# Kernel optimization log

Measured on AMD Instinct MI355X. Metric: run time of the kernel, lower is better.

The kernel has to match this reference:

```python
import jax, jax.numpy as jnp
import numpy as np
from jax import lax

B, C, H, W = 2, 64, 64, 64


def _conv1x1(x, w, b):
    # w: [Cout, Cin], x: [B, Cin, H, W]
    return jnp.einsum('oi,bihw->bohw', w, x) + b[None, :, None, None]


def _conv3x3(x, w, b):
    # w: [Cout, Cin, 3, 3]
    y = lax.conv_general_dilated(x, w, (1, 1), 'SAME',
                                 dimension_numbers=('NCHW', 'OIHW', 'NCHW'))
    return y + b[None, :, None, None]


def _bn(x, s, b, m, v, eps=1e-5):
    # eval-mode batchnorm with running stats
    inv = s / jnp.sqrt(v + eps)
    return x * inv[None, :, None, None] + (b - m * inv)[None, :, None, None]


def _prelu(x, a):
    return jnp.where(x > 0, x, a * x)


def _forward(x, g,
             pam_q_w, pam_q_b, pam_k_w, pam_k_b, pam_v_w, pam_v_b,
             pam_qg_w, pam_qg_b, pam_kg_w, pam_kg_b, gamma_p,
             se_fc1_w, se_fc2_w, gamma_c,
             pconv1_w, pconv1_b, pbn1_s, pbn1_b, pbn1_m, pbn1_v, pprelu1,
             pconv2_w, pconv2_b, pbn2_s, pbn2_b, pbn2_m, pbn2_v, pprelu2,
             cconv1_w, cconv1_b, cbn1_s, cbn1_b, cbn1_m, cbn1_v, cprelu1,
             cconv2_w, cconv2_b, cbn2_s, cbn2_b, cbn2_m, cbn2_v, cprelu2,
             fconv_w, fconv_b, fbn_s, fbn_b, fbn_m, fbn_v, fprelu):
    b, c, h, w = x.shape
    n = h * w
    sm = jax.nn.softmax
    # ---- G_PAM: position attention with guided double softmax ----
    q = _conv1x1(x, pam_q_w, pam_q_b).reshape(b, c, n)
    k = _conv1x1(x, pam_k_w, pam_k_b).reshape(b, c, n)
    v = _conv1x1(x, pam_v_w, pam_v_b).reshape(b, c, n)
    qg = _conv1x1(g, pam_qg_w, pam_qg_b).reshape(b, -1, n)
    kg = _conv1x1(g, pam_kg_w, pam_kg_b).reshape(b, -1, n)
    att = sm(jnp.einsum('bcn,bcm->bnm', q, k), axis=-1)        # [B,N,N]
    att_g = sm(jnp.einsum('bcn,bcm->bnm', qg, kg), axis=-1)    # [B,N,N]
    gatt = sm(jnp.einsum('bnk,bkm->bnm', att, att_g), axis=-1) # [B,N,N]
    pam_o = jnp.einsum('bcm,bnm->bcn', v, gatt).reshape(b, c, h, w)
    pam = gamma_p * pam_o + x
    # ---- pconv head ----
    t = _prelu(_bn(_conv3x3(pam, pconv1_w, pconv1_b), pbn1_s, pbn1_b, pbn1_m, pbn1_v), pprelu1)
    pam2 = _prelu(_bn(_conv1x1(t, pconv2_w, pconv2_b), pbn2_s, pbn2_b, pbn2_m, pbn2_v), pprelu2)
    # ---- G_CAM: channel attention with SE-gated guide ----
    xq = pam2.reshape(b, c, n)
    att_c = sm(jnp.einsum('bcn,bdn->bcd', xq, xq), axis=-1)    # [B,C,C]
    gy = g.mean((2, 3))  # SE: [B,C]
    gy = jax.nn.sigmoid(jnp.einsum('oc,bc->bo', se_fc2_w,
                                   jax.nn.relu(jnp.einsum('rc,bc->br', se_fc1_w, gy))))
    gq = (g * gy[:, :, None, None]).reshape(b, c, n)
    att_cg = sm(jnp.einsum('bcn,bdn->bcd', gq, gq), axis=-1)   # [B,C,C]
    ge = jnp.einsum('bck,bkd->bcd', att_c, att_cg)
    ge = jnp.max(ge, axis=-1, keepdims=True) - ge
    gatt_c = sm(ge, axis=-1)
    cam_o = jnp.einsum('bcd,bdn->bcn', gatt_c, xq).reshape(b, c, h, w)
    cam = gamma_c * cam_o + pam2
    # ---- cconv + fconv heads ----
    t = _prelu(_bn(_conv3x3(cam, cconv1_w, cconv1_b), cbn1_s, cbn1_b, cbn1_m, cbn1_v), cprelu1)
    cam2 = _prelu(_bn(_conv1x1(t, cconv2_w, cconv2_b), cbn2_s, cbn2_b, cbn2_m, cbn2_v), cprelu2)
    final = _prelu(_bn(_conv1x1(cam2, fconv_w, fconv_b), fbn_s, fbn_b, fbn_m, fbn_v), fprelu)
    return final


def setup_inputs() -> dict:
    key = jax.random.key(0)
    keys = iter(jax.random.split(key, 64))
    nk = lambda: next(keys)
    f32 = jnp.float32
    nrm = lambda shape, s=0.1: s * jax.random.normal(nk(), shape, f32)
    d = {}
    d['x'] = jax.random.normal(nk(), (B, C, H, W), f32)
    d['g'] = jax.random.normal(nk(), (B, C, H, W), f32)
    for p in ['pam_q', 'pam_k', 'pam_v', 'pam_qg', 'pam_kg']:
        d[p + '_w'] = nrm((C, C))
        d[p + '_b'] = nrm((C,))
    d['gamma_p'] = jnp.asarray(0.5, f32)
    d['se_fc1_w'] = nrm((C // 2, C))
    d['se_fc2_w'] = nrm((C, C // 2))
    d['gamma_c'] = jnp.asarray(0.5, f32)
    for pre in ['p', 'c']:
        d[pre + 'conv1_w'] = nrm((C, C, 3, 3), 0.05)
        d[pre + 'conv1_b'] = nrm((C,))
        d[pre + 'bn1_s'] = 1.0 + nrm((C,))
        d[pre + 'bn1_b'] = nrm((C,))
        d[pre + 'bn1_m'] = nrm((C,))
        d[pre + 'bn1_v'] = 1.0 + 0.1 * jax.random.uniform(nk(), (C,), f32)
        d[pre + 'prelu1'] = jnp.asarray(0.25, f32)
        d[pre + 'conv2_w'] = nrm((C, C))
        d[pre + 'conv2_b'] = nrm((C,))
        d[pre + 'bn2_s'] = 1.0 + nrm((C,))
        d[pre + 'bn2_b'] = nrm((C,))
        d[pre + 'bn2_m'] = nrm((C,))
        d[pre + 'bn2_v'] = 1.0 + 0.1 * jax.random.uniform(nk(), (C,), f32)
        d[pre + 'prelu2'] = jnp.asarray(0.25, f32)
    d['fconv_w'] = nrm((C, C))
    d['fconv_b'] = nrm((C,))
    d['fbn_s'] = 1.0 + nrm((C,))
    d['fbn_b'] = nrm((C,))
    d['fbn_m'] = nrm((C,))
    d['fbn_v'] = 1.0 + 0.1 * jax.random.uniform(nk(), (C,), f32)
    d['fprelu'] = jnp.asarray(0.25, f32)
    return d


def reference(x, g,
              pam_q_w, pam_q_b, pam_k_w, pam_k_b, pam_v_w, pam_v_b,
              pam_qg_w, pam_qg_b, pam_kg_w, pam_kg_b, gamma_p,
              se_fc1_w, se_fc2_w, gamma_c,
              pconv1_w, pconv1_b, pbn1_s, pbn1_b, pbn1_m, pbn1_v, pprelu1,
              pconv2_w, pconv2_b, pbn2_s, pbn2_b, pbn2_m, pbn2_v, pprelu2,
              cconv1_w, cconv1_b, cbn1_s, cbn1_b, cbn1_m, cbn1_v, cprelu1,
              cconv2_w, cconv2_b, cbn2_s, cbn2_b, cbn2_m, cbn2_v, cprelu2,
              fconv_w, fconv_b, fbn_s, fbn_b, fbn_m, fbn_v, fprelu):
    return _forward(x, g,
                    pam_q_w, pam_q_b, pam_k_w, pam_k_b, pam_v_w, pam_v_b,
                    pam_qg_w, pam_qg_b, pam_kg_w, pam_kg_b, gamma_p,
                    se_fc1_w, se_fc2_w, gamma_c,
                    pconv1_w, pconv1_b, pbn1_s, pbn1_b, pbn1_m, pbn1_v, pprelu1,
                    pconv2_w, pconv2_b, pbn2_s, pbn2_b, pbn2_m, pbn2_v, pprelu2,
                    cconv1_w, cconv1_b, cbn1_s, cbn1_b, cbn1_m, cbn1_v, cprelu1,
                    cconv2_w, cconv2_b, cbn2_s, cbn2_b, cbn2_m, cbn2_v, cprelu2,
                    fconv_w, fconv_b, fbn_s, fbn_b, fbn_m, fbn_v, fprelu)
```

## Files before the change

### kernel.cpp

```cpp
#include <hip/hip_runtime.h>
#include <hip/hip_fp8.h>


typedef float f32x4 __attribute__((ext_vector_type(4)));
typedef __bf16 bf16x8 __attribute__((ext_vector_type(8)));
typedef int int4v __attribute__((ext_vector_type(4)));
typedef int int8v __attribute__((ext_vector_type(8)));
typedef unsigned short ushort8 __attribute__((ext_vector_type(8)));
typedef unsigned char uchar8 __attribute__((ext_vector_type(8)));

#define DI __device__ __forceinline__

DI float bf2f(unsigned short u) { union { unsigned int i; float f; } x; x.i = ((unsigned int)u) << 16; return x.f; }
DI unsigned short f2bf(float f) { union { float f; unsigned int i; } x; x.f = f; unsigned int r = x.i + 0x7fff + ((x.i >> 16) & 1); return (unsigned short)(r >> 16); }
DI unsigned char f2fp8(float f) { __hip_fp8_e4m3 h(f); return (unsigned char)h.__x; }
DI float sane(float x) { return (x > -1e8f) ? ((x < 1e8f) ? x : 1e8f) : -1e8f; }

DI void async16(const unsigned short* g, unsigned short* l) {
    __builtin_amdgcn_global_load_lds(
        (const __attribute__((address_space(1))) void*)g,
        (__attribute__((address_space(3))) void*)l, 16, 0, 0);
}
DI void async16b(const unsigned char* g, unsigned char* l) {
    __builtin_amdgcn_global_load_lds(
        (const __attribute__((address_space(1))) void*)g,
        (__attribute__((address_space(3))) void*)l, 16, 0, 0);
}

__global__ __launch_bounds__(256) void diag_fill(float* __restrict__ out, int n, float val)
{
    int i = blockIdx.x * 256 + threadIdx.x;
    if (i < n) out[i] = val;
}

__global__ __launch_bounds__(256) void gemm_score(
    const unsigned short* __restrict__ A,
    const unsigned short* __restrict__ B,
    unsigned short* __restrict__ C, int N, long abStride, long cStride)
{
    A += (long)blockIdx.z * abStride;
    B += (long)blockIdx.z * abStride;
    C += (long)blockIdx.z * cStride;
    const int tid  = threadIdx.x;
    const int bm   = blockIdx.y, bn = blockIdx.x;
    const int lane = tid & 63, wid = tid >> 6;
    const int wm   = (wid >> 1) * 64, wn = (wid & 1) * 64;
    const int l16  = lane & 15, quad = lane >> 4;

    f32x4 acc[4][4] = {};
    bf16x8 af[2][4], bfr[2][4];
    #pragma unroll
    for (int w = 0; w < 2; w++) {
        #pragma unroll
        for (int i = 0; i < 4; i++)
            af[w][i]  = *(const bf16x8*)&A[(long)(bm * 128 + wm + i * 16 + l16) * 64 + w * 32 + quad * 8];
        #pragma unroll
        for (int j = 0; j < 4; j++)
            bfr[w][j] = *(const bf16x8*)&B[(long)(bn * 128 + wn + j * 16 + l16) * 64 + w * 32 + quad * 8];
    }
    #pragma unroll
    for (int w = 0; w < 2; w++)
        #pragma unroll
        for (int i = 0; i < 4; i++)
            #pragma unroll
            for (int j = 0; j < 4; j++)
                acc[i][j] = __builtin_amdgcn_mfma_f32_16x16x32_bf16(af[w][i], bfr[w][j], acc[i][j], 0, 0, 0);

    #pragma unroll
    for (int i = 0; i < 4; i++) {
        int rb = bm * 128 + wm + i * 16 + quad * 4;
        #pragma unroll
        for (int j = 0; j < 4; j++) {
            int col = bn * 128 + wn + j * 16 + l16;
            #pragma unroll
            for (int r = 0; r < 4; r++)
                C[(long)(rb + r) * N + col] = f2bf(acc[i][j][r]);
        }
    }
}

__global__ __launch_bounds__(256, 3) void gemm_nt(
    const unsigned short* __restrict__ A,
    const unsigned short* __restrict__ B,
    float* __restrict__ C,
    int M, int N, int K, long sA, long sB, long sC)
{
    A += (long)blockIdx.z * sA;
    B += (long)blockIdx.z * sB;
    C += (long)blockIdx.z * sC;
    __shared__ __align__(16) unsigned short As[128 * 32];
    __shared__ __align__(16) unsigned short Bs[128 * 32];
    const int tid  = threadIdx.x;
    const int bn   = blockIdx.x, slice = blockIdx.y;
    const int lane = tid & 63, wid = tid >> 6;
    const int wm   = (wid >> 1) * 64, wn = (wid & 1) * 64;
    const int l16  = lane & 15, quad = lane >> 4;

    f32x4 acc[4][4] = {};

    const int Kc   = K / (int)gridDim.y;
    const int kbeg = slice * Kc;
    const int nIter = Kc / 32;

    const int row0 = tid >> 2,        cp0 = tid & 3;
    const int row1 = (tid + 256) >> 2, cp1 = (tid + 256) & 3;
    int ar0 = row0; if (ar0 > M - 1) ar0 = M - 1;
    int ar1 = row1; if (ar1 > M - 1) ar1 = M - 1;
    const unsigned short* pa0 = &A[(long)ar0 * K + kbeg + ((cp0 ^ (row0 & 3)) * 8)];
    const unsigned short* pa1 = &A[(long)ar1 * K + kbeg + ((cp1 ^ (row1 & 3)) * 8)];
    const unsigned short* pb0 = &B[(long)(bn * 128 + row0) * K + kbeg + ((cp0 ^ (row0 & 3)) * 8)];
    const unsigned short* pb1 = &B[(long)(bn * 128 + row1) * K + kbeg + ((cp1 ^ (row1 & 3)) * 8)];
    unsigned short* la0 = &As[row0 * 32 + cp0 * 8];
    unsigned short* la1 = &As[row1 * 32 + cp1 * 8];
    unsigned short* lb0 = &Bs[row0 * 32 + cp0 * 8];
    unsigned short* lb1 = &Bs[row1 * 32 + cp1 * 8];

    const int sw = (quad ^ (l16 & 3)) * 8;

    for (int it = 0; it < nIter; it++) {
        __syncthreads();
        async16(pa0, la0);
        async16(pa1, la1);
        async16(pb0, lb0);
        async16(pb1, lb1);
        pa0 += 32; pa1 += 32; pb0 += 32; pb1 += 32;
        __syncthreads();
        bf16x8 af[4], bfr[4];
        #pragma unroll
        for (int i = 0; i < 4; i++) af[i]  = *(const bf16x8*)&As[(wm + i * 16 + l16) * 32 + sw];
        #pragma unroll
        for (int j = 0; j < 4; j++) bfr[j] = *(const bf16x8*)&Bs[(wn + j * 16 + l16) * 32 + sw];
        #pragma unroll
        for (int i = 0; i < 4; i++)
            #pragma unroll
            for (int j = 0; j < 4; j++)
                acc[i][j] = __builtin_amdgcn_mfma_f32_16x16x32_bf16(af[i], bfr[j], acc[i][j], 0, 0, 0);
    }

    #pragma unroll
    for (int i = 0; i < 4; i++) {
        int rb = wm + i * 16 + quad * 4;
        #pragma unroll
        for (int j = 0; j < 4; j++) {
            int col = bn * 128 + wn + j * 16 + l16;
            #pragma unroll
            for (int r = 0; r < 4; r++) {
                int row = rb + r;
                if (row < M)
                    C[(long)slice * M * N + (long)row * N + col] = acc[i][j][r];
            }
        }
    }
}

__global__ __launch_bounds__(256, 3) void gemm_p8(
    const unsigned char* __restrict__ A,
    const unsigned char* __restrict__ B,
    unsigned short* __restrict__ C, int N, int K,
    long sA, long sB, long sC)
{
    A += (long)blockIdx.z * sA;
    B += (long)blockIdx.z * sB;
    C += (long)blockIdx.z * sC;
    __shared__ __align__(16) unsigned char As[128 * 128];
    __shared__ __align__(16) unsigned char Bs[128 * 128];
    const int tid  = threadIdx.x;
    const int bm   = blockIdx.y, bn = blockIdx.x;
    const int lane = tid & 63, wid = tid >> 6;
    const int wm   = (wid >> 1) * 64, wn = (wid & 1) * 64;
    const int l16  = lane & 15, quad = lane >> 4;

    f32x4 acc[4][4] = {};

    const unsigned char* pa[4];
    const unsigned char* pb[4];
    unsigned char* la[4];
    unsigned char* lb[4];
    #pragma unroll
    for (int m = 0; m < 4; m++) {
        int ch = tid + m * 256;
        int row = ch >> 3, sp = ch & 7;
        int cp = sp ^ (row & 7);
        pa[m] = &A[(long)(bm * 128 + row) * K + cp * 16];
        pb[m] = &B[(long)(bn * 128 + row) * K + cp * 16];
        la[m] = &As[row * 128 + sp * 16];
        lb[m] = &Bs[row * 128 + sp * 16];
    }

    const int s0 = ((2 * quad) ^ (l16 & 7)) * 16;
    const int s1 = ((2 * quad + 1) ^ (l16 & 7)) * 16;

    const int nIter = K / 128;
    for (int it = 0; it < nIter; it++) {
        __syncthreads();
        #pragma unroll
        for (int m = 0; m < 4; m++) {
            async16b(pa[m], la[m]);
            async16b(pb[m], lb[m]);
            pa[m] += 128; pb[m] += 128;
        }
        __syncthreads();
        int8v bfr[4];
        #pragma unroll
        for (int j = 0; j < 4; j++) {
            const unsigned char* base = &Bs[(wn + j * 16 + l16) * 128];
            int4v v0 = *(const int4v*)(base + s0);
            int4v v1 = *(const int4v*)(base + s1);
            bfr[j][0] = v0[0]; bfr[j][1] = v0[1]; bfr[j][2] = v0[2]; bfr[j][3] = v0[3];
            bfr[j][4] = v1[0]; bfr[j][5] = v1[1]; bfr[j][6] = v1[2]; bfr[j][7] = v1[3];
        }
        #pragma unroll
        for (int i = 0; i < 4; i++) {
            const unsigned char* base = &As[(wm + i * 16 + l16) * 128];
            int4v v0 = *(const int4v*)(base + s0);
            int4v v1 = *(const int4v*)(base + s1);
            int8v af;
            af[0] = v0[0]; af[1] = v0[1]; af[2] = v0[2]; af[3] = v0[3];
            af[4] = v1[0]; af[5] = v1[1]; af[6] = v1[2]; af[7] = v1[3];
            #pragma unroll
            for (int j = 0; j < 4; j++)
                acc[i][j] = __builtin_amdgcn_mfma_scale_f32_16x16x128_f8f6f4(
                    af, bfr[j], acc[i][j],
                    0, 0, 0, 0x7f7f7f7f, 0, 0x7f7f7f7f);
        }
    }

    const float ds = 1.f / 65536.f;
    #pragma unroll
    for (int i = 0; i < 4; i++) {
        int rb = bm * 128 + wm + i * 16 + quad * 4;
        #pragma unroll
        for (int j = 0; j < 4; j++) {
            int col = bn * 128 + wn + j * 16 + l16;
            #pragma unroll
            for (int r = 0; r < 4; r++)
                C[(long)(rb + r) * N + col] = f2bf(acc[i][j][r] * ds);
        }
    }
}

__global__ __launch_bounds__(256) void row_softmax(unsigned short* __restrict__ buf, long bStride)
{
    unsigned short* p = buf + (long)blockIdx.y * bStride + (long)blockIdx.x * 4096;
    const int tid = threadIdx.x, lane = tid & 63, wid = tid >> 6;
    float v[16]; float mx = -1e30f;
    #pragma unroll
    for (int t = 0; t < 16; t++) {
        float x = sane(bf2f(p[t * 256 + tid]));
        v[t] = x; mx = fmaxf(mx, x);
    }
    #pragma unroll
    for (int o = 32; o; o >>= 1) mx = fmaxf(mx, __shfl_xor(mx, o, 64));
    __shared__ float rmax[4], rsum[4];
    if (!lane) rmax[wid] = mx;
    __syncthreads();
    mx = fmaxf(fmaxf(rmax[0], rmax[1]), fmaxf(rmax[2], rmax[3]));
    float s = 0.f;
    #pragma unroll
    for (int t = 0; t < 16; t++) { v[t] = __expf(v[t] - mx); s += v[t]; }
    #pragma unroll
    for (int o = 32; o; o >>= 1) s += __shfl_xor(s, o, 64);
    if (!lane) rsum[wid] = s;
    __syncthreads();
    s = rsum[0] + rsum[1] + rsum[2] + rsum[3];
    float inv = 1.f / s;
    #pragma unroll
    for (int t = 0; t < 16; t++) p[t * 256 + tid] = f2bf(v[t] * inv);
}

__global__ __launch_bounds__(256) void row_softmax_f8(
    const unsigned short* __restrict__ in, unsigned char* __restrict__ out,
    long inStride, long outStride)
{
    const unsigned short* p = in + (long)blockIdx.y * inStride + (long)blockIdx.x * 4096;
    unsigned char* q = out + (long)blockIdx.y * outStride + (long)blockIdx.x * 4096;
    const int tid = threadIdx.x, lane = tid & 63, wid = tid >> 6;
    float v[16]; float mx = -1e30f;
    #pragma unroll
    for (int t = 0; t < 16; t++) {
        float x = sane(bf2f(p[t * 256 + tid]));
        v[t] = x; mx = fmaxf(mx, x);
    }
    #pragma unroll
    for (int o = 32; o; o >>= 1) mx = fmaxf(mx, __shfl_xor(mx, o, 64));
    __shared__ float rmax[4], rsum[4];
    if (!lane) rmax[wid] = mx;
    __syncthreads();
    mx = fmaxf(fmaxf(rmax[0], rmax[1]), fmaxf(rmax[2], rmax[3]));
    float s = 0.f;
    #pragma unroll
    for (int t = 0; t < 16; t++) { v[t] = __expf(v[t] - mx); s += v[t]; }
    #pragma unroll
    for (int o = 32; o; o >>= 1) s += __shfl_xor(s, o, 64);
    if (!lane) rsum[wid] = s;
    __syncthreads();
    s = rsum[0] + rsum[1] + rsum[2] + rsum[3];
    float inv = 256.f / s;
    #pragma unroll
    for (int t = 0; t < 16; t++) q[t * 256 + tid] = f2fp8(v[t] * inv);
}

__global__ __launch_bounds__(256) void colsm_partial(
    const unsigned short* __restrict__ buf,
    float* __restrict__ pmx, float* __restrict__ psum,
    long bufStride, long pStride)
{
    buf  += (long)blockIdx.z * bufStride;
    pmx  += (long)blockIdx.z * pStride;
    psum += (long)blockIdx.z * pStride;
    const int tid = threadIdx.x;
    const int colgrp = tid & 63, rg = tid >> 6;
    const int cbase = blockIdx.x * 512 + colgrp * 8;
    const int r0 = blockIdx.y * 128 + rg * 32;
    const unsigned short* p = buf + (long)r0 * 4096 + cbase;
    float mx[8], s[8];
    #pragma unroll
    for (int j = 0; j < 8; j++) { mx[j] = -1e30f; s[j] = 0.f; }
    for (int r = 0; r < 32; r++) {
        ushort8 v = *(const ushort8*)(p + (long)r * 4096);
        #pragma unroll
        for (int j = 0; j < 8; j++) {
            float x = sane(bf2f(v[j]));
            float nm = fmaxf(mx[j], x);
            s[j] = s[j] * __expf(mx[j] - nm) + __expf(x - nm);
            mx[j] = nm;
        }
    }
    __shared__ float smx[4][512], ssm[4][512];
    #pragma unroll
    for (int j = 0; j < 8; j++) { smx[rg][colgrp * 8 + j] = mx[j]; ssm[rg][colgrp * 8 + j] = s[j]; }
    __syncthreads();
    for (int c = tid; c < 512; c += 256) {
        float M = fmaxf(fmaxf(smx[0][c], smx[1][c]), fmaxf(smx[2][c], smx[3][c]));
        float S = 0.f;
        #pragma unroll
        for (int i = 0; i < 4; i++) S += ssm[i][c] * __expf(smx[i][c] - M);
        int col = blockIdx.x * 512 + c;
        pmx[blockIdx.y * 4096 + col] = M;
        psum[blockIdx.y * 4096 + col] = S;
    }
}

__global__ __launch_bounds__(256) void colsm_combine(
    const float* __restrict__ pmx, const float* __restrict__ psum,
    float* __restrict__ gM, float* __restrict__ gInv,
    long pStride, long gStride)
{
    pmx  += (long)blockIdx.y * pStride;
    psum += (long)blockIdx.y * pStride;
    gM   += (long)blockIdx.y * gStride;
    gInv += (long)blockIdx.y * gStride;
    int col = blockIdx.x * 256 + threadIdx.x;
    float M = -1e30f;
    for (int ch = 0; ch < 32; ch++) M = fmaxf(M, pmx[ch * 4096 + col]);
    float S = 0.f;
    for (int ch = 0; ch < 32; ch++) S += psum[ch * 4096 + col] * __expf(pmx[ch * 4096 + col] - M);
    gM[col] = M;
    gInv[col] = 256.f / S;
}

__global__ __launch_bounds__(256) void colsm_norm_f8(
    const unsigned short* __restrict__ in, unsigned char* __restrict__ out,
    const float* __restrict__ gM, const float* __restrict__ gInv,
    long inStride, long outStride, long gStride)
{
    in   += (long)blockIdx.z * inStride;
    out  += (long)blockIdx.z * outStride;
    gM   += (long)blockIdx.z * gStride;
    gInv += (long)blockIdx.z * gStride;
    const int tid = threadIdx.x;
    const int colgrp = tid & 63, rg = tid >> 6;
    const int cbase = blockIdx.x * 512 + colgrp * 8;
    const int r0 = blockIdx.y * 128 + rg * 32;
    const unsigned short* p = in + (long)r0 * 4096 + cbase;
    unsigned char* q = out + (long)r0 * 4096 + cbase;
    float M[8], inv[8];
    #pragma unroll
    for (int j = 0; j < 8; j++) { M[j] = gM[cbase + j]; inv[j] = gInv[cbase + j]; }
    for (int r = 0; r < 32; r++) {
        ushort8 v = *(const ushort8*)(p + (long)r * 4096);
        uchar8 o;
        #pragma unroll
        for (int j = 0; j < 8; j++) o[j] = f2fp8(__expf(sane(bf2f(v[j])) - M[j]) * inv[j]);
        *(uchar8*)(q + (long)r * 4096) = o;
    }
}

__global__ __launch_bounds__(256) void proj_nc(
    const float* __restrict__ X, const float* __restrict__ W,
    const float* __restrict__ bias, unsigned short* __restrict__ out)
{
    const int b = blockIdx.y, nt = blockIdx.x, tid = threadIdx.x;
    __shared__ float Xs[64][64];
    __shared__ float Ws[64][65];
    __shared__ float Bb[64];
    for (int f = tid; f < 4096; f += 256) {
        int i = f >> 6, n = f & 63;
        Xs[i][n] = X[((long)b * 64 + i) * 4096 + nt * 64 + n];
        Ws[f & 63][f >> 6] = W[f];
    }
    if (tid < 64) Bb[tid] = bias[tid];
    __syncthreads();
    const int c = tid & 63, g = tid >> 6;
    float acc[16];
    #pragma unroll
    for (int j = 0; j < 16; j++) acc[j] = Bb[c];
    for (int i = 0; i < 64; i++) {
        float wv = Ws[i][c];
        #pragma unroll
        for (int j = 0; j < 16; j++) acc[j] += wv * Xs[i][g + 4 * j];
    }
    unsigned short* ob = out + ((long)b * 4096 + nt * 64) * 64;
    #pragma unroll
    for (int j = 0; j < 16; j++) ob[(g + 4 * j) * 64 + c] = f2bf(acc[j]);
}

__global__ __launch_bounds__(256) void proj_cn(
    const float* __restrict__ X, const float* __restrict__ W,
    const float* __restrict__ bias, unsigned short* __restrict__ out)
{
    const int b = blockIdx.y, nt = blockIdx.x, tid = threadIdx.x;
    __shared__ float Xs[64][64];
    __shared__ float Ws[64][64];
    __shared__ float Bb[64];
    for (int f = tid; f < 4096; f += 256) {
        int i = f >> 6, n = f & 63;
        Xs[i][n] = X[((long)b * 64 + i) * 4096 + nt * 64 + n];
        Ws[f >> 6][f & 63] = W[f];
    }
    if (tid < 64) Bb[tid] = bias[tid];
    __syncthreads();
    const int n = tid & 63, g = tid >> 6;
    float acc[16];
    #pragma unroll
    for (int j = 0; j < 16; j++) acc[j] = Bb[g + 4 * j];
    for (int i = 0; i < 64; i++) {
        float xv = Xs[i][n];
        #pragma unroll
        for (int j = 0; j < 16; j++) acc[j] += Ws[g + 4 * j][i] * xv;
    }
    unsigned short* ob = out + ((long)b * 64) * 4096 + nt * 64;
    #pragma unroll
    for (int j = 0; j < 16; j++) ob[(long)(g + 4 * j) * 4096 + n] = f2bf(acc[j]);
}

__global__ __launch_bounds__(256) void combine_pam(
    const float* __restrict__ part, const float* __restrict__ x,
    const float* __restrict__ gammaPtr, float* __restrict__ pam, int nsplit,
    long sPart, long sX)
{
    part += (long)blockIdx.y * sPart;
    x    += (long)blockIdx.y * sX;
    pam  += (long)blockIdx.y * sX;
    int i = blockIdx.x * 256 + threadIdx.x;
    float s = 0.f;
    for (int k = 0; k < nsplit; k++) s += part[(long)k * 262144 + i];
    pam[i] = gammaPtr[0] * s + x[i];
}

__global__ __launch_bounds__(256) void conv3x3_bn(
    const float* __restrict__ X, const float* __restrict__ W9,
    const float* __restrict__ bias,
    const float* __restrict__ bns, const float* __restrict__ bnb,
    const float* __restrict__ bnm, const float* __restrict__ bnv,
    const float* __restrict__ prelu, float* __restrict__ out)
{
    const int b = blockIdx.y, h = blockIdx.x, co0 = blockIdx.z * 16, tid = threadIdx.x;
    __shared__ float Ls[3][64][66];
    __shared__ float ep0[64], ep1[64], ep2[64];
    __shared__ float alpha;
    for (int f = tid; f < 3 * 64 * 64; f += 256) {
        int ky = f >> 12, rem = f & 4095, ci = rem >> 6, w = rem & 63;
        int hh = h + ky - 1;
        Ls[ky][ci][w + 1] = (hh >= 0 && hh < 64) ? X[(((long)b * 64 + ci) * 64 + hh) * 64 + w] : 0.f;
    }
    for (int f = tid; f < 192; f += 256) {
        int ky = f >> 6, ci = f & 63;
        Ls[ky][ci][0] = 0.f; Ls[ky][ci][65] = 0.f;
    }
    if (tid < 64) {
        float inv = bns[tid] * rsqrtf(fmaxf(bnv[tid], 0.f) + 1e-5f);
        ep0[tid] = inv; ep1[tid] = bnb[tid] - bnm[tid] * inv; ep2[tid] = bias[tid];
    }
    if (tid == 0) alpha = prelu[0];
    __syncthreads();
    const int w = tid & 63, g = tid >> 6;
    float acc[4];
    #pragma unroll
    for (int j = 0; j < 4; j++) acc[j] = ep2[co0 + g * 4 + j];
    for (int ci = 0; ci < 64; ci++) {
        float v0 = Ls[0][ci][w], v1 = Ls[0][ci][w + 1], v2 = Ls[0][ci][w + 2];
        float v3 = Ls[1][ci][w], v4 = Ls[1][ci][w + 1], v5 = Ls[1][ci][w + 2];
        float v6 = Ls[2][ci][w], v7 = Ls[2][ci][w + 1], v8 = Ls[2][ci][w + 2];
        #pragma unroll
        for (int j = 0; j < 4; j++) {
            const float* wp = &W9[((co0 + g * 4 + j) * 64 + ci) * 9];
            acc[j] += wp[0] * v0 + wp[1] * v1 + wp[2] * v2
                    + wp[3] * v3 + wp[4] * v4 + wp[5] * v5
                    + wp[6] * v6 + wp[7] * v7 + wp[8] * v8;
        }
    }
    #pragma unroll
    for (int j = 0; j < 4; j++) {
        int co = co0 + g * 4 + j;
        float y = acc[j] * ep0[co] + ep1[co];
        y = y > 0.f ? y : alpha * y;
        out[(((long)b * 64 + co) * 64 + h) * 64 + w] = y;
    }
}

__global__ __launch_bounds__(256) void conv1x1_bn(
    const float* __restrict__ X, const float* __restrict__ W,
    const float* __restrict__ bias,
    const float* __restrict__ bns, const float* __restrict__ bnb,
    const float* __restrict__ bnm, const float* __restrict__ bnv,
    const float* __restrict__ prelu, float* __restrict__ out)
{
    const int b = blockIdx.y, nt = blockIdx.x, tid = threadIdx.x;
    __shared__ float Xs[64][64];
    __shared__ float Ws[64][64];
    __shared__ float ep0[64], ep1[64], ep2[64];
    __shared__ float alpha;
    for (int f = tid; f < 4096; f += 256) {
        int i = f >> 6, n = f & 63;
        Xs[i][n] = X[((long)b * 64 + i) * 4096 + nt * 64 + n];
        Ws[f >> 6][f & 63] = W[f];
    }
    if (tid < 64) {
        float inv = bns[tid] * rsqrtf(fmaxf(bnv[tid], 0.f) + 1e-5f);
        ep0[tid] = inv; ep1[tid] = bnb[tid] - bnm[tid] * inv; ep2[tid] = bias[tid];
    }
    if (tid == 0) alpha = prelu[0];
    __syncthreads();
    const int n = tid & 63, g = tid >> 6;
    float acc[16];
    #pragma unroll
    for (int j = 0; j < 16; j++) acc[j] = ep2[g + 4 * j];
    for (int i = 0; i < 64; i++) {
        float xv = Xs[i][n];
        #pragma unroll
        for (int j = 0; j < 16; j++) acc[j] += Ws[g + 4 * j][i] * xv;
    }
    #pragma unroll
    for (int j = 0; j < 16; j++) {
        int c = g + 4 * j;
        float y = acc[j] * ep0[c] + ep1[c];
        y = y > 0.f ? y : alpha * y;
        out[((long)b * 64 + c) * 4096 + nt * 64 + n] = y;
    }
}

__global__ __launch_bounds__(256) void gram_partial(
    const float* __restrict__ X, float* __restrict__ out)
{
    const int ch = blockIdx.x, b = blockIdx.y, tid = threadIdx.x;
    __shared__ float Xs[64][65];
    for (int f = tid; f < 4096; f += 256) {
        int ci = f >> 6, kk = f & 63;
        Xs[ci][kk] = X[((long)b * 64 + ci) * 4096 + ch * 64 + kk];
    }
    __syncthreads();
    const int d = tid & 63, g = tid >> 6;
    float acc[16] = {};
    for (int kk = 0; kk < 64; kk++) {
        float xd = Xs[d][kk];
        #pragma unroll
        for (int j = 0; j < 16; j++) acc[j] += Xs[g + 4 * j][kk] * xd;
    }
    #pragma unroll
    for (int j = 0; j < 16; j++)
        atomicAdd(&out[((long)b * 64 + (g + 4 * j)) * 64 + d], acc[j]);
}

__global__ __launch_bounds__(256) void se_mean(
    const float* __restrict__ G, float* __restrict__ gy)
{
    const int c = blockIdx.x, b = blockIdx.y, tid = threadIdx.x;
    const int lane = tid & 63, wid = tid >> 6;
    const float* p = G + ((long)b * 64 + c) * 4096;
    float s = 0.f;
    #pragma unroll
    for (int t = 0; t < 4; t++) {
        f32x4 v = *(const f32x4*)(p + (t * 256 + tid) * 4);
        s += v[0] + v[1] + v[2] + v[3];
    }
    #pragma unroll
    for (int o = 32; o; o >>= 1) s += __shfl_xor(s, o, 64);
    __shared__ float ws[4];
    if (!lane) ws[wid] = s;
    __syncthreads();
    if (tid == 0) gy[b * 64 + c] = (ws[0] + ws[1] + ws[2] + ws[3]) * (1.f / 4096.f);
}

__global__ __launch_bounds__(64) void cam_small(
    const float* __restrict__ gramx, const float* __restrict__ gramg,
    const float* __restrict__ gy_in, const float* __restrict__ fc1,
    const float* __restrict__ fc2, float* __restrict__ gattc)
{
    const int b = blockIdx.x, tid = threadIdx.x;
    __shared__ float Ac[64][65], Acg[64][65];
    __shared__ float gyv[64], r1[32], gys[64];
    gyv[tid] = gy_in[b * 64 + tid];
    __syncthreads();
    if (tid < 32) {
        float s = 0.f;
        for (int c = 0; c < 64; c++) s += fc1[tid * 64 + c] * gyv[c];
        r1[tid] = fmaxf(s, 0.f);
    }
    __syncthreads();
    {
        float s = 0.f;
        for (int r = 0; r < 32; r++) s += fc2[tid * 32 + r] * r1[r];
        gys[tid] = 1.f / (1.f + __expf(-sane(s)));
    }
    __syncthreads();
    {
        const float* r = gramx + ((long)b * 64 + tid) * 64;
        float mx = -1e30f;
        for (int d = 0; d < 64; d++) mx = fmaxf(mx, sane(r[d]));
        float s = 0.f;
        for (int d = 0; d < 64; d++) s += __expf(sane(r[d]) - mx);
        float inv = 1.f / s;
        for (int d = 0; d < 64; d++) Ac[tid][d] = __expf(sane(r[d]) - mx) * inv;
    }
    {
        const float* r = gramg + ((long)b * 64 + tid) * 64;
        float gc = gys[tid];
        float mx = -1e30f;
        for (int d = 0; d < 64; d++) mx = fmaxf(mx, sane(gc * gys[d] * r[d]));
        float s = 0.f;
        for (int d = 0; d < 64; d++) s += __expf(sane(gc * gys[d] * r[d]) - mx);
        float inv = 1.f / s;
        for (int d = 0; d < 64; d++) Acg[tid][d] = __expf(sane(gc * gys[d] * r[d]) - mx) * inv;
    }
    __syncthreads();
    float ge[64];
    float mx1 = -1e30f, mn = 1e30f;
    for (int d = 0; d < 64; d++) {
        float s = 0.f;
        for (int k = 0; k < 64; k++) s += Ac[tid][k] * Acg[k][d];
        ge[d] = s;
        mx1 = fmaxf(mx1, s); mn = fminf(mn, s);
    }
    float M2 = mx1 - mn;
    float s = 0.f;
    for (int d = 0; d < 64; d++) s += __expf((mx1 - ge[d]) - M2);
    float inv = 1.f / s;
    for (int d = 0; d < 64; d++)
        gattc[((long)b * 64 + tid) * 64 + d] = __expf((mx1 - ge[d]) - M2) * inv;
}

__global__ __launch_bounds__(256) void cam_apply(
    const float* __restrict__ pam2, const float* __restrict__ gattc,
    const float* __restrict__ gammaPtr, float* __restrict__ cam)
{
    const int b = blockIdx.y, nt = blockIdx.x, tid = threadIdx.x;
    __shared__ float Xs[64][64];
    __shared__ float Gt[64][64];
    for (int f = tid; f < 4096; f += 256) {
        int d = f >> 6, n = f & 63;
        Xs[d][n] = pam2[((long)b * 64 + d) * 4096 + nt * 64 + n];
        Gt[f >> 6][f & 63] = gattc[((long)b * 64 + (f >> 6)) * 64 + (f & 63)];
    }
    __syncthreads();
    const float gamma = gammaPtr[0];
    const int n = tid & 63, g = tid >> 6;
    float acc[16] = {};
    for (int d = 0; d < 64; d++) {
        float xv = Xs[d][n];
        #pragma unroll
        for (int j = 0; j < 16; j++) acc[j] += Gt[g + 4 * j][d] * xv;
    }
    #pragma unroll
    for (int j = 0; j < 16; j++) {
        int c = g + 4 * j;
        cam[((long)b * 64 + c) * 4096 + nt * 64 + n] = gamma * acc[j] + Xs[c][n];
    }
}

extern "C" void kernel_launch(void* const* d_in, const int* in_sizes, int n_in,
                              void* d_out, int out_size, void* d_ws, size_t ws_size,
                              hipStream_t stream)
{
    static const int exp_sizes[51] = {
        524288, 524288,
        4096, 64, 4096, 64, 4096, 64, 4096, 64, 4096, 64,
        1, 2048, 2048, 1,
        36864, 64, 64, 64, 64, 64, 1,
        4096, 64, 64, 64, 64, 64, 1,
        36864, 64, 64, 64, 64, 64, 1,
        4096, 64, 64, 64, 64, 64, 1,
        4096, 64, 64, 64, 64, 64, 1
    };
    bool map_ok = (n_in == 51) && (out_size == 524288);
    if (map_ok) for (int i = 0; i < 51; i++) if (in_sizes[i] != exp_sizes[i]) { map_ok = false; break; }

    const int diag_grid = (out_size + 255) / 256;
    if (!map_ok) {
        diag_fill<<<diag_grid, 256, 0, stream>>>((float*)d_out, out_size, 400.0f);
        return;
    }
    const size_t NEED_FULL = 121000000;
    if (ws_size < NEED_FULL) {
        float code = (ws_size >= 88000000) ? 100.0f : (ws_size >= 55000000 ? 200.0f : 300.0f);
        diag_fill<<<diag_grid, 256, 0, stream>>>((float*)d_out, out_size, code);
        return;
    }
    const bool big = (ws_size >= 248000000);
    const int nb = big ? 2 : 1;
    const long NN = 4096L * 4096;

    auto IN = [&](int i) { return (const float*)d_in[i]; };
    const float* X = IN(0);
    const float* G = IN(1);

    char* wp_ = (char*)d_ws;
    auto alloc = [&](size_t bytes) -> void* {
        void* p = (void*)wp_;
        wp_ += (bytes + 255) & ~(size_t)255;
        return p;
    };
    unsigned short* qT   = (unsigned short*)alloc(2L * 4096 * 64 * 2);
    unsigned short* kT   = (unsigned short*)alloc(2L * 4096 * 64 * 2);
    unsigned short* qgT  = (unsigned short*)alloc(2L * 4096 * 64 * 2);
    unsigned short* kgT  = (unsigned short*)alloc(2L * 4096 * 64 * 2);
    unsigned short* vC   = (unsigned short*)alloc(2L * 64 * 4096 * 2);
    float* part  = (float*)alloc((8L * nb) * 64 * 4096 * 4);
    float* pam   = (float*)alloc(2L * 64 * 4096 * 4);
    float* tbuf  = (float*)alloc(2L * 64 * 4096 * 4);
    float* pam2  = (float*)alloc(2L * 64 * 4096 * 4);
    float* cam   = (float*)alloc(2L * 64 * 4096 * 4);
    float* gramx = (float*)alloc(2L * 64 * 64 * 4);
    float* gramg = (float*)alloc(2L * 64 * 64 * 4);
    float* gy    = (float*)alloc(2L * 64 * 4);
    float* gattc = (float*)alloc(2L * 64 * 64 * 4);
    float* pmx   = (float*)alloc((32L * nb) * 4096 * 4);
    float* psum  = (float*)alloc((32L * nb) * 4096 * 4);
    float* gM    = (float*)alloc(4096L * nb * 4);
    float* gInv  = (float*)alloc(4096L * nb * 4);
    unsigned short* pbuf   = (unsigned short*)alloc(NN * 2 * nb);
    unsigned short* attS   = (unsigned short*)alloc(NN * 2 * nb);
    unsigned char*  attF8  = (unsigned char*)alloc(NN * nb);
    unsigned char*  attgF8 = (unsigned char*)alloc(NN * nb);
    float* cam2 = tbuf;

    proj_nc<<<dim3(64, 2), 256, 0, stream>>>(X, IN(2),  IN(3),  qT);
    proj_nc<<<dim3(64, 2), 256, 0, stream>>>(X, IN(4),  IN(5),  kT);
    proj_nc<<<dim3(64, 2), 256, 0, stream>>>(G, IN(8),  IN(9),  qgT);
    proj_nc<<<dim3(64, 2), 256, 0, stream>>>(G, IN(10), IN(11), kgT);
    proj_cn<<<dim3(64, 2), 256, 0, stream>>>(X, IN(6),  IN(7),  vC);

    const long abStr = 4096L * 64;
    const long pStr  = big ? NN : 0;
    const long pmStr = big ? 32L * 4096 : 0;
    const long gStr  = big ? 4096L : 0;
    for (int b = 0; b < 2; b += nb) {
        const unsigned short* qTb  = qT  + (long)b * abStr;
        const unsigned short* kTb  = kT  + (long)b * abStr;
        const unsigned short* qgTb = qgT + (long)b * abStr;
        const unsigned short* kgTb = kgT + (long)b * abStr;
        gemm_score<<<dim3(32, 32, nb), 256, 0, stream>>>(qTb,  kTb,  pbuf, 4096, abStr, pStr);
        gemm_score<<<dim3(32, 32, nb), 256, 0, stream>>>(kgTb, qgTb, attS, 4096, abStr, pStr);
        row_softmax_f8<<<dim3(4096, nb), 256, 0, stream>>>(pbuf, attF8, pStr, pStr);
        colsm_partial<<<dim3(8, 32, nb), 256, 0, stream>>>(attS, pmx, psum, pStr, pmStr);
        colsm_combine<<<dim3(16, nb), 256, 0, stream>>>(pmx, psum, gM, gInv, pmStr, gStr);
        colsm_norm_f8<<<dim3(8, 32, nb), 256, 0, stream>>>(attS, attgF8, gM, gInv, pStr, pStr, gStr);
        gemm_p8<<<dim3(32, 32, nb), 256, 0, stream>>>(attF8, attgF8, pbuf, 4096, 4096, pStr, pStr, pStr);
        row_softmax<<<dim3(4096, nb), 256, 0, stream>>>(pbuf, pStr);
        gemm_nt<<<dim3(32, 8, nb), 256, 0, stream>>>(vC + (long)b * abStr, pbuf, part,
                                                     64, 4096, 4096,
                                                     abStr, pStr, big ? 8L * 262144 : 0);
        combine_pam<<<dim3(1024, nb), 256, 0, stream>>>(part, X + (long)b * 262144, IN(12),
                                                        pam + (long)b * 262144, 8,
                                                        big ? 8L * 262144 : 0,
                                                        big ? 262144L : 0);
    }

    conv3x3_bn<<<dim3(64, 2, 4), 256, 0, stream>>>(pam, IN(16), IN(17), IN(18), IN(19), IN(20), IN(21), IN(22), tbuf);
    conv1x1_bn<<<dim3(64, 2), 256, 0, stream>>>(tbuf, IN(23), IN(24), IN(25), IN(26), IN(27), IN(28), IN(29), pam2);

    diag_fill<<<64, 256, 0, stream>>>(gramx, 16384, 0.0f);
    gram_partial<<<dim3(64, 2), 256, 0, stream>>>(pam2, gramx);
    gram_partial<<<dim3(64, 2), 256, 0, stream>>>(G,    gramg);
    se_mean<<<dim3(64, 2), 256, 0, stream>>>(G, gy);
    cam_small<<<2, 64, 0, stream>>>(gramx, gramg, gy, IN(13), IN(14), gattc);
    cam_apply<<<dim3(64, 2), 256, 0, stream>>>(pam2, gattc, IN(15), cam);

    conv3x3_bn<<<dim3(64, 2, 4), 256, 0, stream>>>(cam, IN(30), IN(31), IN(32), IN(33), IN(34), IN(35), IN(36), pam);
    conv1x1_bn<<<dim3(64, 2), 256, 0, stream>>>(pam, IN(37), IN(38), IN(39), IN(40), IN(41), IN(42), IN(43), cam2);
    conv1x1_bn<<<dim3(64, 2), 256, 0, stream>>>(cam2, IN(44), IN(45), IN(46), IN(47), IN(48), IN(49), IN(50), (float*)d_out);
}
```

Measured before the change: 671.8 us.

## Deepen fp8 GEMM K-tile and fuse projection, softmax-combine and SE-mean kernels

```diff
diff --git a/kernel.cpp b/kernel.cpp
--- a/kernel.cpp
+++ b/kernel.cpp
@@ -153,7 +153,7 @@
     }
 }
 
-__global__ __launch_bounds__(256, 3) void gemm_p8(
+__global__ __launch_bounds__(256, 2) void gemm_p8(
     const unsigned char* __restrict__ A,
     const unsigned char* __restrict__ B,
     unsigned short* __restrict__ C, int N, int K,
@@ -162,8 +162,8 @@
     A += (long)blockIdx.z * sA;
     B += (long)blockIdx.z * sB;
     C += (long)blockIdx.z * sC;
-    __shared__ __align__(16) unsigned char As[128 * 128];
-    __shared__ __align__(16) unsigned char Bs[128 * 128];
+    __shared__ __align__(16) unsigned char As[128 * 256];
+    __shared__ __align__(16) unsigned char Bs[128 * 256];
     const int tid  = threadIdx.x;
     const int bm   = blockIdx.y, bn = blockIdx.x;
     const int lane = tid & 63, wid = tid >> 6;
@@ -172,56 +172,53 @@
 
     f32x4 acc[4][4] = {};
 
-    const unsigned char* pa[4];
-    const unsigned char* pb[4];
-    unsigned char* la[4];
-    unsigned char* lb[4];
-    #pragma unroll
-    for (int m = 0; m < 4; m++) {
-        int ch = tid + m * 256;
-        int row = ch >> 3, sp = ch & 7;
-        int cp = sp ^ (row & 7);
-        pa[m] = &A[(long)(bm * 128 + row) * K + cp * 16];
-        pb[m] = &B[(long)(bn * 128 + row) * K + cp * 16];
-        la[m] = &As[row * 128 + sp * 16];
-        lb[m] = &Bs[row * 128 + sp * 16];
-    }
-
-    const int s0 = ((2 * quad) ^ (l16 & 7)) * 16;
-    const int s1 = ((2 * quad + 1) ^ (l16 & 7)) * 16;
-
-    const int nIter = K / 128;
+    const int srow = tid >> 4;
+    const int sp   = tid & 15;
+    const int cp   = sp ^ (srow & 15);
+    const unsigned char* pa = &A[(long)(bm * 128 + srow) * K + cp * 16];
+    const unsigned char* pb = &B[(long)(bn * 128 + srow) * K + cp * 16];
+    unsigned char* la = &As[srow * 256 + sp * 16];
+    unsigned char* lb = &Bs[srow * 256 + sp * 16];
+    const long gstep = 16L * K;
+
+    const int nIter = K / 256;
     for (int it = 0; it < nIter; it++) {
         __syncthreads();
         #pragma unroll
-        for (int m = 0; m < 4; m++) {
-            async16b(pa[m], la[m]);
-            async16b(pb[m], lb[m]);
-            pa[m] += 128; pb[m] += 128;
-        }
+        for (int m = 0; m < 8; m++) {
+            async16b(pa + m * gstep, la + m * 4096);
+            async16b(pb + m * gstep, lb + m * 4096);
+        }
+        pa += 256; pb += 256;
         __syncthreads();
-        int8v bfr[4];
-        #pragma unroll
-        for (int j = 0; j < 4; j++) {
-            const unsigned char* base = &Bs[(wn + j * 16 + l16) * 128];
-            int4v v0 = *(const int4v*)(base + s0);
-            int4v v1 = *(const int4v*)(base + s1);
-            bfr[j][0] = v0[0]; bfr[j][1] = v0[1]; bfr[j][2] = v0[2]; bfr[j][3] = v0[3];
-            bfr[j][4] = v1[0]; bfr[j][5] = v1[1]; bfr[j][6] = v1[2]; bfr[j][7] = v1[3];
-        }
-        #pragma unroll
-        for (int i = 0; i < 4; i++) {
-            const unsigned char* base = &As[(wm + i * 16 + l16) * 128];
-            int4v v0 = *(const int4v*)(base + s0);
-            int4v v1 = *(const int4v*)(base + s1);
-            int8v af;
-            af[0] = v0[0]; af[1] = v0[1]; af[2] = v0[2]; af[3] = v0[3];
-            af[4] = v1[0]; af[5] = v1[1]; af[6] = v1[2]; af[7] = v1[3];
-            #pragma unroll
-            for (int j = 0; j < 4; j++)
-                acc[i][j] = __builtin_amdgcn_mfma_scale_f32_16x16x128_f8f6f4(
-                    af, bfr[j], acc[i][j],
-                    0, 0, 0, 0x7f7f7f7f, 0, 0x7f7f7f7f);
+        #pragma unroll
+        for (int h = 0; h < 2; h++) {
+            const int c0 = h * 8 + 2 * quad;
+            const int s0 = (c0 ^ (l16 & 15)) * 16;
+            const int s1 = ((c0 + 1) ^ (l16 & 15)) * 16;
+            int8v bfr[4];
+            #pragma unroll
+            for (int j = 0; j < 4; j++) {
+                const unsigned char* base = &Bs[(wn + j * 16 + l16) * 256];
+                int4v v0 = *(const int4v*)(base + s0);
+                int4v v1 = *(const int4v*)(base + s1);
+                bfr[j][0] = v0[0]; bfr[j][1] = v0[1]; bfr[j][2] = v0[2]; bfr[j][3] = v0[3];
+                bfr[j][4] = v1[0]; bfr[j][5] = v1[1]; bfr[j][6] = v1[2]; bfr[j][7] = v1[3];
+            }
+            #pragma unroll
+            for (int i = 0; i < 4; i++) {
+                const unsigned char* base = &As[(wm + i * 16 + l16) * 256];
+                int4v v0 = *(const int4v*)(base + s0);
+                int4v v1 = *(const int4v*)(base + s1);
+                int8v af;
+                af[0] = v0[0]; af[1] = v0[1]; af[2] = v0[2]; af[3] = v0[3];
+                af[4] = v1[0]; af[5] = v1[1]; af[6] = v1[2]; af[7] = v1[3];
+                #pragma unroll
+                for (int j = 0; j < 4; j++)
+                    acc[i][j] = __builtin_amdgcn_mfma_scale_f32_16x16x128_f8f6f4(
+                        af, bfr[j], acc[i][j],
+                        0, 0, 0, 0x7f7f7f7f, 0, 0x7f7f7f7f);
+            }
         }
     }
 
@@ -341,33 +338,15 @@
     }
 }
 
-__global__ __launch_bounds__(256) void colsm_combine(
-    const float* __restrict__ pmx, const float* __restrict__ psum,
-    float* __restrict__ gM, float* __restrict__ gInv,
-    long pStride, long gStride)
-{
-    pmx  += (long)blockIdx.y * pStride;
-    psum += (long)blockIdx.y * pStride;
-    gM   += (long)blockIdx.y * gStride;
-    gInv += (long)blockIdx.y * gStride;
-    int col = blockIdx.x * 256 + threadIdx.x;
-    float M = -1e30f;
-    for (int ch = 0; ch < 32; ch++) M = fmaxf(M, pmx[ch * 4096 + col]);
-    float S = 0.f;
-    for (int ch = 0; ch < 32; ch++) S += psum[ch * 4096 + col] * __expf(pmx[ch * 4096 + col] - M);
-    gM[col] = M;
-    gInv[col] = 256.f / S;
-}
-
 __global__ __launch_bounds__(256) void colsm_norm_f8(
     const unsigned short* __restrict__ in, unsigned char* __restrict__ out,
-    const float* __restrict__ gM, const float* __restrict__ gInv,
-    long inStride, long outStride, long gStride)
+    const float* __restrict__ pmx, const float* __restrict__ psum,
+    long inStride, long outStride, long pStride)
 {
     in   += (long)blockIdx.z * inStride;
     out  += (long)blockIdx.z * outStride;
-    gM   += (long)blockIdx.z * gStride;
-    gInv += (long)blockIdx.z * gStride;
+    pmx  += (long)blockIdx.z * pStride;
+    psum += (long)blockIdx.z * pStride;
     const int tid = threadIdx.x;
     const int colgrp = tid & 63, rg = tid >> 6;
     const int cbase = blockIdx.x * 512 + colgrp * 8;
@@ -376,7 +355,21 @@
     unsigned char* q = out + (long)r0 * 4096 + cbase;
     float M[8], inv[8];
     #pragma unroll
-    for (int j = 0; j < 8; j++) { M[j] = gM[cbase + j]; inv[j] = gInv[cbase + j]; }
+    for (int j = 0; j < 8; j++) M[j] = -1e30f;
+    for (int ch = 0; ch < 32; ch++) {
+        #pragma unroll
+        for (int j = 0; j < 8; j++) M[j] = fmaxf(M[j], pmx[ch * 4096 + cbase + j]);
+    }
+    float S[8];
+    #pragma unroll
+    for (int j = 0; j < 8; j++) S[j] = 0.f;
+    for (int ch = 0; ch < 32; ch++) {
+        #pragma unroll
+        for (int j = 0; j < 8; j++)
+            S[j] += psum[ch * 4096 + cbase + j] * __expf(pmx[ch * 4096 + cbase + j] - M[j]);
+    }
+    #pragma unroll
+    for (int j = 0; j < 8; j++) inv[j] = 256.f / S[j];
     for (int r = 0; r < 32; r++) {
         ushort8 v = *(const ushort8*)(p + (long)r * 4096);
         uchar8 o;
@@ -386,62 +379,118 @@
     }
 }
 
-__global__ __launch_bounds__(256) void proj_nc(
-    const float* __restrict__ X, const float* __restrict__ W,
-    const float* __restrict__ bias, unsigned short* __restrict__ out)
+__global__ __launch_bounds__(256) void proj_x3(
+    const float* __restrict__ X,
+    const float* __restrict__ Wq, const float* __restrict__ bq,
+    const float* __restrict__ Wk, const float* __restrict__ bk,
+    const float* __restrict__ Wv, const float* __restrict__ bv,
+    unsigned short* __restrict__ qT, unsigned short* __restrict__ kT,
+    unsigned short* __restrict__ vC)
 {
     const int b = blockIdx.y, nt = blockIdx.x, tid = threadIdx.x;
     __shared__ float Xs[64][64];
-    __shared__ float Ws[64][65];
-    __shared__ float Bb[64];
+    __shared__ float Wqs[64][65];
+    __shared__ float Wks[64][65];
+    __shared__ float Wvs[64][64];
+    __shared__ float Bq[64], Bk[64], Bv[64];
     for (int f = tid; f < 4096; f += 256) {
         int i = f >> 6, n = f & 63;
         Xs[i][n] = X[((long)b * 64 + i) * 4096 + nt * 64 + n];
-        Ws[f & 63][f >> 6] = W[f];
-    }
-    if (tid < 64) Bb[tid] = bias[tid];
+        Wqs[f & 63][f >> 6] = Wq[f];
+        Wks[f & 63][f >> 6] = Wk[f];
+        Wvs[f >> 6][f & 63] = Wv[f];
+    }
+    if (tid < 64) { Bq[tid] = bq[tid]; Bk[tid] = bk[tid]; Bv[tid] = bv[tid]; }
     __syncthreads();
     const int c = tid & 63, g = tid >> 6;
-    float acc[16];
-    #pragma unroll
-    for (int j = 0; j < 16; j++) acc[j] = Bb[c];
-    for (int i = 0; i < 64; i++) {
-        float wv = Ws[i][c];
-        #pragma unroll
-        for (int j = 0; j < 16; j++) acc[j] += wv * Xs[i][g + 4 * j];
-    }
-    unsigned short* ob = out + ((long)b * 4096 + nt * 64) * 64;
-    #pragma unroll
-    for (int j = 0; j < 16; j++) ob[(g + 4 * j) * 64 + c] = f2bf(acc[j]);
-}
-
-__global__ __launch_bounds__(256) void proj_cn(
-    const float* __restrict__ X, const float* __restrict__ W,
-    const float* __restrict__ bias, unsigned short* __restrict__ out)
+    {
+        float acc[16];
+        #pragma unroll
+        for (int j = 0; j < 16; j++) acc[j] = Bq[c];
+        for (int i = 0; i < 64; i++) {
+            float wv = Wqs[i][c];
+            #pragma unroll
+            for (int j = 0; j < 16; j++) acc[j] += wv * Xs[i][g + 4 * j];
+        }
+        unsigned short* ob = qT + ((long)b * 4096 + nt * 64) * 64;
+        #pragma unroll
+        for (int j = 0; j < 16; j++) ob[(g + 4 * j) * 64 + c] = f2bf(acc[j]);
+    }
+    {
+        float acc[16];
+        #pragma unroll
+        for (int j = 0; j < 16; j++) acc[j] = Bk[c];
+        for (int i = 0; i < 64; i++) {
+            float wv = Wks[i][c];
+            #pragma unroll
+            for (int j = 0; j < 16; j++) acc[j] += wv * Xs[i][g + 4 * j];
+        }
+        unsigned short* ob = kT + ((long)b * 4096 + nt * 64) * 64;
+        #pragma unroll
+        for (int j = 0; j < 16; j++) ob[(g + 4 * j) * 64 + c] = f2bf(acc[j]);
+    }
+    {
+        const int n = tid & 63, gg = tid >> 6;
+        float acc[16];
+        #pragma unroll
+        for (int j = 0; j < 16; j++) acc[j] = Bv[gg + 4 * j];
+        for (int i = 0; i < 64; i++) {
+            float xv = Xs[i][n];
+            #pragma unroll
+            for (int j = 0; j < 16; j++) acc[j] += Wvs[gg + 4 * j][i] * xv;
+        }
+        unsigned short* ob = vC + ((long)b * 64) * 4096 + nt * 64;
+        #pragma unroll
+        for (int j = 0; j < 16; j++) ob[(long)(gg + 4 * j) * 4096 + n] = f2bf(acc[j]);
+    }
+}
+
+__global__ __launch_bounds__(256) void proj_g2(
+    const float* __restrict__ G,
+    const float* __restrict__ Wq, const float* __restrict__ bq,
+    const float* __restrict__ Wk, const float* __restrict__ bk,
+    unsigned short* __restrict__ qgT, unsigned short* __restrict__ kgT)
 {
     const int b = blockIdx.y, nt = blockIdx.x, tid = threadIdx.x;
     __shared__ float Xs[64][64];
-    __shared__ float Ws[64][64];
-    __shared__ float Bb[64];
+    __shared__ float Wqs[64][65];
+    __shared__ float Wks[64][65];
+    __shared__ float Bq[64], Bk[64];
     for (int f = tid; f < 4096; f += 256) {
         int i = f >> 6, n = f & 63;
-        Xs[i][n] = X[((long)b * 64 + i) * 4096 + nt * 64 + n];
-        Ws[f >> 6][f & 63] = W[f];
-    }
-    if (tid < 64) Bb[tid] = bias[tid];
-    __syncthreads();
-    const int n = tid & 63, g = tid >> 6;
-    float acc[16];
-    #pragma unroll
-    for (int j = 0; j < 16; j++) acc[j] = Bb[g + 4 * j];
-    for (int i = 0; i < 64; i++) {
-        float xv = Xs[i][n];
-        #pragma unroll
-        for (int j = 0; j < 16; j++) acc[j] += Ws[g + 4 * j][i] * xv;
-    }
-    unsigned short* ob = out + ((long)b * 64) * 4096 + nt * 64;
-    #pragma unroll
-    for (int j = 0; j < 16; j++) ob[(long)(g + 4 * j) * 4096 + n] = f2bf(acc[j]);
+        Xs[i][n] = G[((long)b * 64 + i) * 4096 + nt * 64 + n];
+        Wqs[f & 63][f >> 6] = Wq[f];
+        Wks[f & 63][f >> 6] = Wk[f];
+    }
+    if (tid < 64) { Bq[tid] = bq[tid]; Bk[tid] = bk[tid]; }
+    __syncthreads();
+    const int c = tid & 63, g = tid >> 6;
+    {
+        float acc[16];
+        #pragma unroll
+        for (int j = 0; j < 16; j++) acc[j] = Bq[c];
+        for (int i = 0; i < 64; i++) {
+            float wv = Wqs[i][c];
+            #pragma unroll
+            for (int j = 0; j < 16; j++) acc[j] += wv * Xs[i][g + 4 * j];
+        }
+        unsigned short* ob = qgT + ((long)b * 4096 + nt * 64) * 64;
+        #pragma unroll
+        for (int j = 0; j < 16; j++) ob[(g + 4 * j) * 64 + c] = f2bf(acc[j]);
+    }
+    {
+        float acc[16];
+        #pragma unroll
+        for (int j = 0; j < 16; j++) acc[j] = Bk[c];
+        for (int i = 0; i < 64; i++) {
+            float wv = Wks[i][c];
+            #pragma unroll
+            for (int j = 0; j < 16; j++) acc[j] += wv * Xs[i][g + 4 * j];
+        }
+        unsigned short* ob = kgT + ((long)b * 4096 + nt * 64) * 64;
+        #pragma unroll
+        for (int j = 0; j < 16; j++) ob[(g + 4 * j) * 64 + c] = f2bf(acc[j]);
+    }
 }
 
 __global__ __launch_bounds__(256) void combine_pam(
@@ -551,7 +600,7 @@
 }
 
 __global__ __launch_bounds__(256) void gram_partial(
-    const float* __restrict__ X, float* __restrict__ out)
+    const float* __restrict__ X, float* __restrict__ out, float* __restrict__ gy)
 {
     const int ch = blockIdx.x, b = blockIdx.y, tid = threadIdx.x;
     __shared__ float Xs[64][65];
@@ -570,26 +619,11 @@
     #pragma unroll
     for (int j = 0; j < 16; j++)
         atomicAdd(&out[((long)b * 64 + (g + 4 * j)) * 64 + d], acc[j]);
-}
-
-__global__ __launch_bounds__(256) void se_mean(
-    const float* __restrict__ G, float* __restrict__ gy)
-{
-    const int c = blockIdx.x, b = blockIdx.y, tid = threadIdx.x;
-    const int lane = tid & 63, wid = tid >> 6;
-    const float* p = G + ((long)b * 64 + c) * 4096;
-    float s = 0.f;
-    #pragma unroll
-    for (int t = 0; t < 4; t++) {
-        f32x4 v = *(const f32x4*)(p + (t * 256 + tid) * 4);
-        s += v[0] + v[1] + v[2] + v[3];
-    }
-    #pragma unroll
-    for (int o = 32; o; o >>= 1) s += __shfl_xor(s, o, 64);
-    __shared__ float ws[4];
-    if (!lane) ws[wid] = s;
-    __syncthreads();
-    if (tid == 0) gy[b * 64 + c] = (ws[0] + ws[1] + ws[2] + ws[3]) * (1.f / 4096.f);
+    if (gy && tid < 64) {
+        float s = 0.f;
+        for (int kk = 0; kk < 64; kk++) s += Xs[tid][kk];
+        atomicAdd(&gy[b * 64 + tid], s);
+    }
 }
 
 __global__ __launch_bounds__(64) void cam_small(
@@ -600,7 +634,7 @@
     const int b = blockIdx.x, tid = threadIdx.x;
     __shared__ float Ac[64][65], Acg[64][65];
     __shared__ float gyv[64], r1[32], gys[64];
-    gyv[tid] = gy_in[b * 64 + tid];
+    gyv[tid] = gy_in[b * 64 + tid] * (1.f / 4096.f);
     __syncthreads();
     if (tid < 32) {
         float s = 0.f;
@@ -736,24 +770,18 @@
     float* gattc = (float*)alloc(2L * 64 * 64 * 4);
     float* pmx   = (float*)alloc((32L * nb) * 4096 * 4);
     float* psum  = (float*)alloc((32L * nb) * 4096 * 4);
-    float* gM    = (float*)alloc(4096L * nb * 4);
-    float* gInv  = (float*)alloc(4096L * nb * 4);
     unsigned short* pbuf   = (unsigned short*)alloc(NN * 2 * nb);
     unsigned short* attS   = (unsigned short*)alloc(NN * 2 * nb);
     unsigned char*  attF8  = (unsigned char*)alloc(NN * nb);
     unsigned char*  attgF8 = (unsigned char*)alloc(NN * nb);
     float* cam2 = tbuf;
 
-    proj_nc<<<dim3(64, 2), 256, 0, stream>>>(X, IN(2),  IN(3),  qT);
-    proj_nc<<<dim3(64, 2), 256, 0, stream>>>(X, IN(4),  IN(5),  kT);
-    proj_nc<<<dim3(64, 2), 256, 0, stream>>>(G, IN(8),  IN(9),  qgT);
-    proj_nc<<<dim3(64, 2), 256, 0, stream>>>(G, IN(10), IN(11), kgT);
-    proj_cn<<<dim3(64, 2), 256, 0, stream>>>(X, IN(6),  IN(7),  vC);
+    proj_x3<<<dim3(64, 2), 256, 0, stream>>>(X, IN(2), IN(3), IN(4), IN(5), IN(6), IN(7), qT, kT, vC);
+    proj_g2<<<dim3(64, 2), 256, 0, stream>>>(G, IN(8), IN(9), IN(10), IN(11), qgT, kgT);
 
     const long abStr = 4096L * 64;
     const long pStr  = big ? NN : 0;
     const long pmStr = big ? 32L * 4096 : 0;
-    const long gStr  = big ? 4096L : 0;
     for (int b = 0; b < 2; b += nb) {
         const unsigned short* qTb  = qT  + (long)b * abStr;
         const unsigned short* kTb  = kT  + (long)b * abStr;
@@ -763,8 +791,7 @@
         gemm_score<<<dim3(32, 32, nb), 256, 0, stream>>>(kgTb, qgTb, attS, 4096, abStr, pStr);
         row_softmax_f8<<<dim3(4096, nb), 256, 0, stream>>>(pbuf, attF8, pStr, pStr);
         colsm_partial<<<dim3(8, 32, nb), 256, 0, stream>>>(attS, pmx, psum, pStr, pmStr);
-        colsm_combine<<<dim3(16, nb), 256, 0, stream>>>(pmx, psum, gM, gInv, pmStr, gStr);
-        colsm_norm_f8<<<dim3(8, 32, nb), 256, 0, stream>>>(attS, attgF8, gM, gInv, pStr, pStr, gStr);
+        colsm_norm_f8<<<dim3(8, 32, nb), 256, 0, stream>>>(attS, attgF8, pmx, psum, pStr, pStr, pmStr);
         gemm_p8<<<dim3(32, 32, nb), 256, 0, stream>>>(attF8, attgF8, pbuf, 4096, 4096, pStr, pStr, pStr);
         row_softmax<<<dim3(4096, nb), 256, 0, stream>>>(pbuf, pStr);
         gemm_nt<<<dim3(32, 8, nb), 256, 0, stream>>>(vC + (long)b * abStr, pbuf, part,
@@ -779,10 +806,9 @@
     conv3x3_bn<<<dim3(64, 2, 4), 256, 0, stream>>>(pam, IN(16), IN(17), IN(18), IN(19), IN(20), IN(21), IN(22), tbuf);
     conv1x1_bn<<<dim3(64, 2), 256, 0, stream>>>(tbuf, IN(23), IN(24), IN(25), IN(26), IN(27), IN(28), IN(29), pam2);
 
-    diag_fill<<<64, 256, 0, stream>>>(gramx, 16384, 0.0f);
-    gram_partial<<<dim3(64, 2), 256, 0, stream>>>(pam2, gramx);
-    gram_partial<<<dim3(64, 2), 256, 0, stream>>>(G,    gramg);
-    se_mean<<<dim3(64, 2), 256, 0, stream>>>(G, gy);
+    diag_fill<<<65, 256, 0, stream>>>(gramx, 16384 + 128, 0.0f);
+    gram_partial<<<dim3(64, 2), 256, 0, stream>>>(pam2, gramx, nullptr);
+    gram_partial<<<dim3(64, 2), 256, 0, stream>>>(G,    gramg, gy);
     cam_small<<<2, 64, 0, stream>>>(gramx, gramg, gy, IN(13), IN(14), gattc);
     cam_apply<<<dim3(64, 2), 256, 0, stream>>>(pam2, gattc, IN(15), cam);
 
```

Measured after the change: 674.9 us. Within noise of the previous version (+0.5%).
